# Optimization experiments

Measured on AMD Instinct MI355X. Metric: run time of the kernel, lower is better.

Reference implementation:

```python
import jax, jax.numpy as jnp
import numpy as np


def _lstm_scan(xs, W_ih, W_hh, b, h0, c0):
    """Run an LSTMCell over time. xs: [T, B, D]; returns (hs [T,B,H], h_T, c_T).
    PyTorch LSTMCell gate order: i, f, g, o; b = b_ih + b_hh fused."""
    H = h0.shape[-1]

    def step(carry, x_t):
        h, c = carry
        gates = x_t @ W_ih.T + h @ W_hh.T + b  # [B, 4H]
        i, f, g, o = jnp.split(gates, 4, axis=-1)
        i = jax.nn.sigmoid(i)
        f = jax.nn.sigmoid(f)
        g = jnp.tanh(g)
        o = jax.nn.sigmoid(o)
        c_new = f * c + i * g
        h_new = o * jnp.tanh(c_new)
        return (h_new, c_new), h_new

    (h_T, c_T), hs = jax.lax.scan(step, (h0, c0), xs)
    return hs, h_T, c_T


def setup_inputs() -> dict:
    key = jax.random.key(0)
    ks = jax.random.split(key, 7)
    B, T, F, H = 64, 512, 256, 1024
    s = lambda fan_in: np.sqrt(2.0) * np.sqrt(6.0 / (4 * H + fan_in))  # xavier_uniform gain=sqrt(2)
    return {
        "x": jax.random.normal(ks[0], (B, T, F), dtype=jnp.float32),
        "W_ih_e": jax.random.uniform(ks[1], (4 * H, F), jnp.float32, -s(F), s(F)),
        "W_hh_e": jax.random.uniform(ks[2], (4 * H, H), jnp.float32, -s(H), s(H)),
        "b_e": jnp.zeros((4 * H,), jnp.float32),
        "W_ih_d": jax.random.uniform(ks[3], (4 * H, H), jnp.float32, -s(H), s(H)),
        "W_hh_d": jax.random.uniform(ks[4], (4 * H, H), jnp.float32, -s(H), s(H)),
        "b_d": jnp.zeros((4 * H,), jnp.float32),
        "W_out": jax.random.uniform(ks[5], (F, H), jnp.float32, -s(F), s(F)),
        "b_out": jnp.zeros((F,), jnp.float32),
    }


def reference(x, W_ih_e, W_hh_e, b_e, W_ih_d, W_hh_d, b_d, W_out, b_out):
    B, T, F = x.shape
    H = W_hh_e.shape[1]
    xs = jnp.swapaxes(x, 0, 1)  # [T, B, F] time-major
    h0 = jnp.zeros((B, H), x.dtype)
    c0 = jnp.zeros((B, H), x.dtype)
    # Encoder: LSTMCell(F, H), collect per-step hidden states
    enc_hs, h_T, c_T = _lstm_scan(xs, W_ih_e, W_hh_e, b_e, h0, c0)  # [T, B, H]
    # Decoder: LSTMCell(H, H) over encoder hidden states, seeded with final (h, c)
    dec_hs, _, _ = _lstm_scan(enc_hs, W_ih_d, W_hh_d, b_d, h_T, c_T)  # [T, B, H]
    # Output projection H -> F
    out = jnp.einsum('tbh,fh->tbf', dec_hs, W_out) + b_out
    return jnp.swapaxes(out, 0, 1)  # [B, T, F]
```

## Files before the change

### kernel.cpp

```cpp
#include <hip/hip_runtime.h>
#include <math.h>

#define TT 512
#define BB 64
#define FF 256
#define HH 1024
#define NBLK 256
#define NCHE 5
#define NCHD 8

typedef __attribute__((ext_vector_type(8))) short short8;
typedef __attribute__((ext_vector_type(4))) float f32x4;

__device__ __forceinline__ unsigned short f2bf(float f) {
    unsigned u = __float_as_uint(f);
    u += 0x7FFFu + ((u >> 16) & 1u);
    return (unsigned short)(u >> 16);
}
__device__ __forceinline__ float bf2f(unsigned short u) {
    return __uint_as_float((unsigned)u << 16);
}

__global__ __launch_bounds__(256) void k_cast_x(const float* __restrict__ x,
                                                unsigned short* __restrict__ xB) {
    int t = blockIdx.x;
    #pragma unroll
    for (int i = 0; i < 16; ++i) {
        int id = threadIdx.x + i * 256;
        int b  = id >> 6;
        int f4 = (id & 63) << 2;
        float4 v = *(const float4*)(x + ((size_t)b * TT + t) * FF + f4);
        ushort4 o;
        o.x = f2bf(v.x); o.y = f2bf(v.y); o.z = f2bf(v.z); o.w = f2bf(v.w);
        *(ushort4*)(xB + ((size_t)t * BB + b) * FF + f4) = o;
    }
}

__global__ __launch_bounds__(256) void k_wcast(const float* __restrict__ in,
                                               unsigned short* __restrict__ out,
                                               int n4) {
    int stride = gridDim.x * 256;
    for (int i = blockIdx.x * 256 + threadIdx.x; i < n4; i += stride) {
        float4 v = ((const float4*)in)[i];
        ushort4 o;
        o.x = f2bf(v.x); o.y = f2bf(v.y); o.z = f2bf(v.z); o.w = f2bf(v.w);
        ((ushort4*)out)[i] = o;
    }
}

__device__ __forceinline__ void publish(unsigned* __restrict__ flags,
                                        int widx, unsigned val) {
    asm volatile("s_waitcnt vmcnt(0)" ::: "memory");
    if ((threadIdx.x & 63) == 0)
        __hip_atomic_store(flags + widx, val, __ATOMIC_RELAXED,
                           __HIP_MEMORY_SCOPE_AGENT);
}

__device__ __forceinline__ void waitall(const unsigned* __restrict__ flags,
                                        int lane, unsigned tgt) {
    const unsigned long long* f2 = (const unsigned long long*)flags;
    for (;;) {
        bool ok = true;
        #pragma unroll
        for (int k = 0; k < 8; ++k) {
            unsigned long long v = __hip_atomic_load(f2 + lane + 64 * k,
                                                     __ATOMIC_RELAXED,
                                                     __HIP_MEMORY_SCOPE_AGENT);
            ok &= ((unsigned)v >= tgt) && ((unsigned)(v >> 32) >= tgt);
        }
        if (__all(ok)) break;
        __builtin_amdgcn_s_sleep(2);
    }
    asm volatile("" ::: "memory");
}

template <int NCH, int NPRE>
__device__ __forceinline__ void lstm_step(
    const short8* __restrict__ sW,
    const unsigned short* __restrict__ A1, int K1,
    const unsigned short* __restrict__ A2, int K2, int C1,
    const f32x4 bias, float& creg,
    unsigned short* __restrict__ hOut,
    unsigned* __restrict__ flags, int tgt, int widx, unsigned pub,
    int lane, int q, int n, int j0, int u, int b)
{
    short8 av[3][8];
    auto aload = [&](short8* dst, int c) {
        const unsigned short* ap = (c < C1)
            ? A1 + (size_t)b * K1 + (size_t)c * 256
            : A2 + (size_t)b * K2 + (size_t)(c - C1) * 256;
        ap += q * 8;
        #pragma unroll
        for (int f = 0; f < 8; ++f) dst[f] = *(const short8*)(ap + f * 32);
    };

    aload(av[0], 0);
    if (NCH > 1 && NPRE > 1) aload(av[1], 1);

    if (tgt > 0) waitall(flags, lane, (unsigned)tgt);

    if (NCH > 1 && NPRE <= 1) aload(av[1], 1);

    f32x4 accA = {0.f, 0.f, 0.f, 0.f};
    f32x4 accB = {0.f, 0.f, 0.f, 0.f};
    #pragma unroll
    for (int c = 0; c < NCH; ++c) {
        if (c + 2 < NCH) aload(av[(c + 2) % 3], c + 2);
        const short8* cur = av[c % 3];
        #pragma unroll
        for (int f = 0; f < 8; ++f) {
            short8 wv = sW[(c * 8 + f) * 64 + lane];
            if (f & 1) accB = __builtin_amdgcn_mfma_f32_16x16x32_bf16(wv, cur[f], accB, 0, 0, 0);
            else       accA = __builtin_amdgcn_mfma_f32_16x16x32_bf16(wv, cur[f], accA, 0, 0, 0);
        }
    }
    f32x4 acc = accA + accB;

    float pi = acc[0] + bias[0];
    float pf = acc[1] + bias[1];
    float pg = acc[2] + bias[2];
    float po = acc[3] + bias[3];
    float iv = 1.f / (1.f + __expf(-pi));
    float fv = 1.f / (1.f + __expf(-pf));
    float gv = tanhf(pg);
    float ov = 1.f / (1.f + __expf(-po));
    float cn = fv * creg + iv * gv;
    creg = cn;
    float hn = ov * tanhf(cn);

    unsigned hv = (unsigned)f2bf(hn);
    unsigned v0 = (unsigned)__shfl((int)hv, n);
    unsigned v1 = (unsigned)__shfl((int)hv, n + 16);
    unsigned v2 = (unsigned)__shfl((int)hv, n + 32);
    unsigned v3 = (unsigned)__shfl((int)hv, n + 48);
    if (q == 0) {
        unsigned long long pk = (unsigned long long)(v0 | (v1 << 16)) |
                                ((unsigned long long)(v2 | (v3 << 16)) << 32);
        __hip_atomic_store((unsigned long long*)(hOut + (size_t)b * HH + j0), pk,
                           __ATOMIC_RELAXED, __HIP_MEMORY_SCOPE_AGENT);
    }
    if (pub) publish(flags, widx, pub);
}

__global__ __launch_bounds__(256, 1) void k_lstm_persist(
    const unsigned short* __restrict__ xB,
    const unsigned short* __restrict__ WihE,
    const unsigned short* __restrict__ WhhE,
    const float* __restrict__ bE,
    const unsigned short* __restrict__ WihD,
    const unsigned short* __restrict__ WhhD,
    const float* __restrict__ bD,
    unsigned short* __restrict__ encB,
    unsigned short* __restrict__ decR,
    unsigned* __restrict__ flags)
{
    __shared__ short8 sWe[NCHE * 8 * 64];
    __shared__ short8 sWd[NCHD * 8 * 64];

    const int tid  = threadIdx.x;
    const int lane = tid & 63;
    const int w    = tid >> 6;
    const int q    = lane >> 4;
    const int n    = lane & 15;
    const int j0   = blockIdx.x * 4;
    const int rrow = (n & 3) * HH + j0 + (n >> 2);
    const size_t SB = (size_t)BB * HH;
    const int widx = blockIdx.x * 4 + w;

    #pragma unroll
    for (int i = 0; i < 2 * NCHE; ++i) {
        int g = i * 4 + w;
        int c = g >> 3, f = g & 7;
        const unsigned short* Wp; int Ks; int cl;
        if (c < 1) { Wp = WihE; Ks = FF; cl = c; }
        else       { Wp = WhhE; Ks = HH; cl = c - 1; }
        sWe[g * 64 + lane] =
            *(const short8*)(Wp + (size_t)rrow * Ks + (size_t)cl * 256 + f * 32 + q * 8);
    }
    #pragma unroll
    for (int i = 0; i < 2 * NCHD; ++i) {
        int g = i * 4 + w;
        int c = g >> 3, f = g & 7;
        const unsigned short* Wp; int cl;
        if (c < 4) { Wp = WihD; cl = c; }
        else       { Wp = WhhD; cl = c - 4; }
        sWd[g * 64 + lane] =
            *(const short8*)(Wp + (size_t)rrow * HH + (size_t)cl * 256 + f * 32 + q * 8);
    }
    __syncthreads();

    const int u = j0 + q;
    const int b = w * 16 + n;
    const f32x4 biasE = {bE[u], bE[HH + u], bE[2 * HH + u], bE[3 * HH + u]};
    const f32x4 biasD = {bD[u], bD[HH + u], bD[2 * HH + u], bD[3 * HH + u]};

    float creg = 0.f;

    lstm_step<1, 1>(sWe, xB, FF, xB, FF, 1, biasE, creg,
                    encB, flags, 0, widx, 1u, lane, q, n, j0, u, b);
    for (int t = 1; t < TT; ++t) {
        lstm_step<NCHE, 1>(sWe, xB + (size_t)t * BB * FF, FF,
                           encB + (size_t)(t - 1) * SB, HH, 1,
                           biasE, creg, encB + (size_t)t * SB,
                           flags, t, widx, (unsigned)(t + 1),
                           lane, q, n, j0, u, b);
    }

    for (int t = 0; t < TT; ++t) {
        const unsigned short* A2 = (t == 0) ? encB + (size_t)(TT - 1) * SB
                                            : decR + (size_t)(t - 1) * SB;
        unsigned pub = (t == TT - 1) ? 0u : (unsigned)(TT + t + 1);
        lstm_step<NCHD, 2>(sWd, encB + (size_t)t * SB, HH, A2, HH, 4,
                           biasD, creg, decR + (size_t)t * SB,
                           flags, TT + t, widx, pub,
                           lane, q, n, j0, u, b);
    }
}

__global__ __launch_bounds__(256) void k_out_proj_r(
    const unsigned short* __restrict__ decR,
    const float* __restrict__ Wout,
    const float* __restrict__ bout,
    float* __restrict__ out)
{
    int t  = blockIdx.x;
    int fg = blockIdx.y;
    const int lane = threadIdx.x & 63;
    const int wv   = __builtin_amdgcn_readfirstlane(threadIdx.x >> 6);
    const int f0   = fg * 64 + wv * 16;
    const unsigned short* a = decR + ((size_t)t * BB + lane) * HH;

    float acc[16];
    #pragma unroll
    for (int i = 0; i < 16; ++i) acc[i] = bout[f0 + i];

    for (int k8 = 0; k8 < HH / 8; ++k8) {
        short8 hv8 = *(const short8*)(a + k8 * 8);
        #pragma unroll
        for (int uu = 0; uu < 8; ++uu) {
            float hv = bf2f((unsigned short)hv8[uu]);
            #pragma unroll
            for (int i = 0; i < 16; ++i)
                acc[i] = fmaf(Wout[(size_t)(f0 + i) * HH + k8 * 8 + uu], hv, acc[i]);
        }
    }

    float* op = out + ((size_t)lane * TT + t) * FF + f0;
    #pragma unroll
    for (int i = 0; i < 16; i += 4) {
        float4 v = make_float4(acc[i], acc[i + 1], acc[i + 2], acc[i + 3]);
        *(float4*)(op + i) = v;
    }
}

template <int NCH>
__global__ __launch_bounds__(256) void k_step_lds(
    const unsigned short* __restrict__ A1, const unsigned short* __restrict__ W1, int K1,
    const unsigned short* __restrict__ A2, const unsigned short* __restrict__ W2, int K2,
    int C1,
    const float* __restrict__ bias,
    float* __restrict__ Cbuf,
    unsigned short* __restrict__ hOut,
    float* __restrict__ chunkOut)
{
    __shared__ short8 sW[NCH * 8 * 64];

    const int tid  = threadIdx.x;
    const int lane = tid & 63;
    const int w    = tid >> 6;
    const int q    = lane >> 4;
    const int n    = lane & 15;
    const int j0   = blockIdx.x * 4;
    const int rrow = (n & 3) * HH + j0 + (n >> 2);

    short8 av[3][8];

    auto aload = [&](short8* dst, int c) {
        const unsigned short* ap = (c < C1)
            ? A1 + (size_t)(w * 16 + n) * K1 + (size_t)c * 256
            : A2 + (size_t)(w * 16 + n) * K2 + (size_t)(c - C1) * 256;
        ap += q * 8;
        #pragma unroll
        for (int f = 0; f < 8; ++f) dst[f] = *(const short8*)(ap + f * 32);
    };

    aload(av[0], 0);
    if (NCH > 1) aload(av[1], 1);

    #pragma unroll
    for (int i = 0; i < 2 * NCH; ++i) {
        int g = i * 4 + w;
        int c = g >> 3, f = g & 7;
        const unsigned short* Wp; int Ks; int cl;
        if (c < C1) { Wp = W1; Ks = K1; cl = c; }
        else        { Wp = W2; Ks = K2; cl = c - C1; }
        sW[g * 64 + lane] =
            *(const short8*)(Wp + (size_t)rrow * Ks + (size_t)cl * 256 + f * 32 + q * 8);
    }
    __syncthreads();

    f32x4 accA = {0.f, 0.f, 0.f, 0.f};
    f32x4 accB = {0.f, 0.f, 0.f, 0.f};
    #pragma unroll
    for (int c = 0; c < NCH; ++c) {
        if (c + 2 < NCH) aload(av[(c + 2) % 3], c + 2);
        const short8* cur = av[c % 3];
        #pragma unroll
        for (int f = 0; f < 8; ++f) {
            short8 wv = sW[(c * 8 + f) * 64 + lane];
            if (f & 1) accB = __builtin_amdgcn_mfma_f32_16x16x32_bf16(wv, cur[f], accB, 0, 0, 0);
            else       accA = __builtin_amdgcn_mfma_f32_16x16x32_bf16(wv, cur[f], accA, 0, 0, 0);
        }
    }
    f32x4 acc = accA + accB;

    const int u = j0 + q;
    const int b = w * 16 + n;
    float pi = acc[0] + bias[u];
    float pf = acc[1] + bias[HH + u];
    float pg = acc[2] + bias[2 * HH + u];
    float po = acc[3] + bias[3 * HH + u];
    float iv = 1.f / (1.f + __expf(-pi));
    float fv = 1.f / (1.f + __expf(-pf));
    float gv = tanhf(pg);
    float ov = 1.f / (1.f + __expf(-po));
    size_t cix = (size_t)u * BB + b;
    float c  = Cbuf[cix];
    float cn = fv * c + iv * gv;
    Cbuf[cix] = cn;
    float hn = ov * tanhf(cn);
    hOut[(size_t)b * HH + u] = f2bf(hn);
    if (chunkOut) chunkOut[cix] = hn;
}

__device__ __forceinline__ void seg_f32(const unsigned short* __restrict__ ap0,
                                        const float* __restrict__ wp0,
                                        int nch, f32x4& acc) {
    const unsigned short* ap = ap0;
    const float* wp = wp0;
    #pragma unroll 2
    for (int c = 0; c < nch; ++c) {
        float4 wa = *(const float4*)wp;
        float4 wb = *(const float4*)(wp + 4);
        short8 av = *(const short8*)ap;
        short8 wv;
        wv[0] = (short)f2bf(wa.x); wv[1] = (short)f2bf(wa.y);
        wv[2] = (short)f2bf(wa.z); wv[3] = (short)f2bf(wa.w);
        wv[4] = (short)f2bf(wb.x); wv[5] = (short)f2bf(wb.y);
        wv[6] = (short)f2bf(wb.z); wv[7] = (short)f2bf(wb.w);
        acc = __builtin_amdgcn_mfma_f32_16x16x32_bf16(wv, av, acc, 0, 0, 0);
        ap += 32; wp += 32;
    }
}

__global__ __launch_bounds__(256) void k_step_f32w(
    const unsigned short* __restrict__ A1, const float* __restrict__ W1, int K1,
    const unsigned short* __restrict__ A2, const float* __restrict__ W2, int K2,
    const float* __restrict__ bias,
    float* __restrict__ Cbuf, unsigned short* __restrict__ hOut,
    float* __restrict__ chunkOut)
{
    const int tid  = threadIdx.x;
    const int lane = tid & 63;
    const int w    = tid >> 6;
    const int q    = lane >> 4;
    const int n    = lane & 15;
    const int j0   = blockIdx.x * 4;
    const int rrow = (n & 3) * HH + j0 + (n >> 2);

    f32x4 acc = {0.f, 0.f, 0.f, 0.f};
    seg_f32(A1 + (size_t)(w * 16 + n) * K1 + q * 8,
            W1 + (size_t)rrow * K1 + q * 8, K1 >> 5, acc);
    if (K2)
        seg_f32(A2 + (size_t)(w * 16 + n) * HH + q * 8,
                W2 + (size_t)rrow * HH + q * 8, HH >> 5, acc);

    const int u = j0 + q;
    const int b = w * 16 + n;
    float pi = acc[0] + bias[u];
    float pf = acc[1] + bias[HH + u];
    float pg = acc[2] + bias[2 * HH + u];
    float po = acc[3] + bias[3 * HH + u];
    float iv = 1.f / (1.f + __expf(-pi));
    float fv = 1.f / (1.f + __expf(-pf));
    float gv = tanhf(pg);
    float ov = 1.f / (1.f + __expf(-po));
    size_t cix = (size_t)u * BB + b;
    float c  = Cbuf[cix];
    float cn = fv * c + iv * gv;
    Cbuf[cix] = cn;
    float hn = ov * tanhf(cn);
    hOut[(size_t)b * HH + u] = f2bf(hn);
    if (chunkOut) chunkOut[cix] = hn;
}

__global__ __launch_bounds__(256) void k_out_proj(
    const float* __restrict__ chunk,
    const float* __restrict__ Wout,
    const float* __restrict__ bout,
    float* __restrict__ out,
    int t0)
{
    int tl = blockIdx.x;
    int t  = t0 + tl;
    int fg = blockIdx.y;
    const int lane = threadIdx.x & 63;
    const int wv   = __builtin_amdgcn_readfirstlane(threadIdx.x >> 6);
    const int f0   = fg * 64 + wv * 16;
    const float* a = chunk + (size_t)tl * HH * BB;

    float acc[16];
    #pragma unroll
    for (int i = 0; i < 16; ++i) acc[i] = bout[f0 + i];

    for (int k = 0; k < HH; k += 4) {
        #pragma unroll
        for (int u = 0; u < 4; ++u) {
            float hv = a[(size_t)(k + u) * BB + lane];
            #pragma unroll
            for (int i = 0; i < 16; ++i)
                acc[i] = fmaf(Wout[(size_t)(f0 + i) * HH + k + u], hv, acc[i]);
        }
    }

    float* op = out + ((size_t)lane * TT + t) * FF + f0;
    #pragma unroll
    for (int i = 0; i < 16; i += 4) {
        float4 v = make_float4(acc[i], acc[i + 1], acc[i + 2], acc[i + 3]);
        *(float4*)(op + i) = v;
    }
}

extern "C" void kernel_launch(void* const* d_in, const int* in_sizes, int n_in,
                              void* d_out, int out_size, void* d_ws, size_t ws_size,
                              hipStream_t stream) {
    const float* x     = (const float*)d_in[0];
    const float* Wih_e = (const float*)d_in[1];
    const float* Whh_e = (const float*)d_in[2];
    const float* b_e   = (const float*)d_in[3];
    const float* Wih_d = (const float*)d_in[4];
    const float* Whh_d = (const float*)d_in[5];
    const float* b_d   = (const float*)d_in[6];
    const float* Wout  = (const float*)d_in[7];
    const float* bout  = (const float*)d_in[8];
    float* out = (float*)d_out;

    const size_t SB = (size_t)BB * HH;

    unsigned short* xB = (unsigned short*)d_out;

    {
        char* p = (char*)d_ws;
        unsigned* flags = (unsigned*)p; p += 4096;
        unsigned short* encB  = (unsigned short*)p; p += (size_t)TT * SB * 2;
        unsigned short* decR  = (unsigned short*)p; p += (size_t)TT * SB * 2;
        unsigned short* WihEb = (unsigned short*)p; p += (size_t)4 * HH * FF * 2;
        unsigned short* WhhEb = (unsigned short*)p; p += (size_t)4 * HH * HH * 2;
        unsigned short* WihDb = (unsigned short*)p; p += (size_t)4 * HH * HH * 2;
        unsigned short* WhhDb = (unsigned short*)p; p += (size_t)4 * HH * HH * 2;
        size_t need = (size_t)(p - (char*)d_ws);

        if (ws_size >= need) {
            hipMemsetAsync(flags, 0, 4096, stream);
            k_cast_x<<<TT, 256, 0, stream>>>(x, xB);
            k_wcast<<<1024, 256, 0, stream>>>(Wih_e, WihEb, 4 * HH * FF / 4);
            k_wcast<<<1024, 256, 0, stream>>>(Whh_e, WhhEb, 4 * HH * HH / 4);
            k_wcast<<<1024, 256, 0, stream>>>(Wih_d, WihDb, 4 * HH * HH / 4);
            k_wcast<<<1024, 256, 0, stream>>>(Whh_d, WhhDb, 4 * HH * HH / 4);

            void* args[] = {
                (void*)&xB, (void*)&WihEb, (void*)&WhhEb, (void*)&b_e,
                (void*)&WihDb, (void*)&WhhDb, (void*)&b_d,
                (void*)&encB, (void*)&decR, (void*)&flags};
            hipLaunchCooperativeKernel((const void*)k_lstm_persist,
                                       dim3(NBLK), dim3(256), args, 0, stream);

            k_out_proj_r<<<dim3(TT, 4), 256, 0, stream>>>(decR, Wout, bout, out);
            return;
        }
    }

    char* p = (char*)d_ws;
    unsigned short* encB  = (unsigned short*)p; p += (size_t)TT * SB * 2;
    unsigned short* dech0 = (unsigned short*)p; p += SB * 2;
    unsigned short* dech1 = (unsigned short*)p; p += SB * 2;
    float* cbuf = (float*)p; p += SB * 4;
    size_t used  = (size_t)(p - (char*)d_ws);
    size_t avail = ws_size > used ? ws_size - used : 0;

    const size_t WE_B = ((size_t)4 * HH * FF + (size_t)4 * HH * HH) * 2;
    const size_t WD_B = ((size_t)4 * HH * HH) * 2 * 2;
    const size_t CH8  = (size_t)8 * SB * 4;

    bool wbAll = (avail >= WE_B + WD_B + CH8);
    bool wbEnc = wbAll || (avail >= WE_B + CH8);

    unsigned short *WihEb = 0, *WhhEb = 0, *WihDb = 0, *WhhDb = 0;
    if (wbEnc) {
        WihEb = (unsigned short*)p; p += (size_t)4 * HH * FF * 2;
        WhhEb = (unsigned short*)p; p += (size_t)4 * HH * HH * 2;
        avail -= WE_B;
    }
    if (wbAll) {
        WihDb = (unsigned short*)p; p += (size_t)4 * HH * HH * 2;
        WhhDb = (unsigned short*)p; p += (size_t)4 * HH * HH * 2;
        avail -= WD_B;
    }
    int C = 8;
    if      (avail >= (size_t)64 * SB * 4) C = 64;
    else if (avail >= (size_t)32 * SB * 4) C = 32;
    else if (avail >= (size_t)16 * SB * 4) C = 16;
    float* chunk = (float*)p;

    hipMemsetAsync(cbuf, 0, SB * 4, stream);
    k_cast_x<<<TT, 256, 0, stream>>>(x, xB);
    if (wbEnc) {
        k_wcast<<<1024, 256, 0, stream>>>(Wih_e, WihEb, 4 * HH * FF / 4);
        k_wcast<<<1024, 256, 0, stream>>>(Whh_e, WhhEb, 4 * HH * HH / 4);
    }
    if (wbAll) {
        k_wcast<<<1024, 256, 0, stream>>>(Wih_d, WihDb, 4 * HH * HH / 4);
        k_wcast<<<1024, 256, 0, stream>>>(Whh_d, WhhDb, 4 * HH * HH / 4);
    }

    for (int t = 0; t < TT; ++t) {
        const unsigned short* A1 = xB + (size_t)t * BB * FF;
        const unsigned short* A2 = t ? encB + (size_t)(t - 1) * SB : (unsigned short*)0;
        unsigned short* hOut = encB + (size_t)t * SB;
        if (wbEnc) {
            if (t == 0)
                k_step_lds<1><<<256, 256, 0, stream>>>(A1, WihEb, FF, A2, WhhEb, HH,
                                                       1, b_e, cbuf, hOut, (float*)0);
            else
                k_step_lds<5><<<256, 256, 0, stream>>>(A1, WihEb, FF, A2, WhhEb, HH,
                                                       1, b_e, cbuf, hOut, (float*)0);
        } else {
            k_step_f32w<<<256, 256, 0, stream>>>(A1, Wih_e, FF, A2, Whh_e,
                                                 t ? HH : 0, b_e, cbuf, hOut, (float*)0);
        }
    }

    for (int t = 0; t < TT; ++t) {
        const unsigned short* A1 = encB + (size_t)t * SB;
        const unsigned short* A2 = (t == 0) ? encB + (size_t)(TT - 1) * SB
                                            : ((t & 1) ? dech1 : dech0);
        unsigned short* hOut = ((t + 1) & 1) ? dech1 : dech0;
        int l = t & (C - 1);
        float* ch = chunk + (size_t)l * SB;
        if (wbAll)
            k_step_lds<8><<<256, 256, 0, stream>>>(A1, WihDb, HH, A2, WhhDb, HH,
                                                   4, b_d, cbuf, hOut, ch);
        else
            k_step_f32w<<<256, 256, 0, stream>>>(A1, Wih_d, FF, A2, Whh_d, HH,
                                                 b_d, cbuf, hOut, ch);
        if (l == C - 1)
            k_out_proj<<<dim3(C, 4), 256, 0, stream>>>(chunk, Wout, bout, out,
                                                       t - (C - 1));
    }
}
```

Measured before the change: 12.05 ms.

## Add hierarchical flag aggregation and compute input-side MFMAs before barrier wait

Each block gains a fifth warp. In every 16th block that warp acts as an aggregator: it watches 64 per-warp progress flags and writes the combined epoch into 8 mirrored pages. Compute warps then poll one small mirror line instead of scanning all 1024 flags. The lstm_step also runs all input-dependent MFMA chunks (x for the encoder, encoder hidden state for the decoder) before waiting on the barrier, overlapping that work with the sync. The trade-off is an extra relay hop of latency per step and extra resident warps.

```diff
diff --git a/kernel.cpp b/kernel.cpp
--- a/kernel.cpp
+++ b/kernel.cpp
@@ -56,32 +56,48 @@
                            __HIP_MEMORY_SCOPE_AGENT);
 }
 
-__device__ __forceinline__ void waitall(const unsigned* __restrict__ flags,
-                                        int lane, unsigned tgt) {
-    const unsigned long long* f2 = (const unsigned long long*)flags;
+__device__ __forceinline__ void waitall16(const unsigned* __restrict__ mir,
+                                          int mpage, int lane, unsigned tgt) {
+    const unsigned long long* line =
+        (const unsigned long long*)(mir + mpage * 64);
     for (;;) {
-        bool ok = true;
-        #pragma unroll
-        for (int k = 0; k < 8; ++k) {
-            unsigned long long v = __hip_atomic_load(f2 + lane + 64 * k,
-                                                     __ATOMIC_RELAXED,
-                                                     __HIP_MEMORY_SCOPE_AGENT);
-            ok &= ((unsigned)v >= tgt) && ((unsigned)(v >> 32) >= tgt);
-        }
+        unsigned long long v = __hip_atomic_load(line + (lane & 7),
+                                                 __ATOMIC_RELAXED,
+                                                 __HIP_MEMORY_SCOPE_AGENT);
+        bool ok = ((unsigned)v >= tgt) && ((unsigned)(v >> 32) >= tgt);
         if (__all(ok)) break;
-        __builtin_amdgcn_s_sleep(2);
+        __builtin_amdgcn_s_sleep(1);
     }
     asm volatile("" ::: "memory");
 }
 
-template <int NCH, int NPRE>
+__device__ __forceinline__ void aggregator(unsigned* __restrict__ flags,
+                                           unsigned* __restrict__ mir,
+                                           int g, int lane) {
+    for (unsigned e = 1; e <= 2u * TT - 1; ++e) {
+        for (;;) {
+            unsigned v = __hip_atomic_load(flags + g * 64 + lane,
+                                           __ATOMIC_RELAXED,
+                                           __HIP_MEMORY_SCOPE_AGENT);
+            if (__all(v >= e)) break;
+            __builtin_amdgcn_s_sleep(1);
+        }
+        if (lane < 8)
+            __hip_atomic_store(mir + lane * 64 + g, e, __ATOMIC_RELAXED,
+                               __HIP_MEMORY_SCOPE_AGENT);
+        asm volatile("s_waitcnt vmcnt(0)" ::: "memory");
+    }
+}
+
+template <int NCH, int C1>
 __device__ __forceinline__ void lstm_step(
     const short8* __restrict__ sW,
     const unsigned short* __restrict__ A1, int K1,
-    const unsigned short* __restrict__ A2, int K2, int C1,
+    const unsigned short* __restrict__ A2, int K2,
     const f32x4 bias, float& creg,
     unsigned short* __restrict__ hOut,
-    unsigned* __restrict__ flags, int tgt, int widx, unsigned pub,
+    unsigned* __restrict__ flags, unsigned* __restrict__ mir,
+    int tgt, int widx, unsigned pub, int mpage,
     int lane, int q, int n, int j0, int u, int b)
 {
     short8 av[3][8];
@@ -94,24 +110,38 @@
         for (int f = 0; f < 8; ++f) dst[f] = *(const short8*)(ap + f * 32);
     };
 
-    aload(av[0], 0);
-    if (NCH > 1 && NPRE > 1) aload(av[1], 1);
-
-    if (tgt > 0) waitall(flags, lane, (unsigned)tgt);
-
-    if (NCH > 1 && NPRE <= 1) aload(av[1], 1);
-
     f32x4 accA = {0.f, 0.f, 0.f, 0.f};
     f32x4 accB = {0.f, 0.f, 0.f, 0.f};
-    #pragma unroll
-    for (int c = 0; c < NCH; ++c) {
-        if (c + 2 < NCH) aload(av[(c + 2) % 3], c + 2);
+
+    aload(av[0], 0);
+    if (C1 > 1) aload(av[1], 1);
+    #pragma unroll
+    for (int c = 0; c < C1; ++c) {
+        if (c + 2 < C1) aload(av[(c + 2) % 3], c + 2);
         const short8* cur = av[c % 3];
         #pragma unroll
         for (int f = 0; f < 8; ++f) {
             short8 wv = sW[(c * 8 + f) * 64 + lane];
             if (f & 1) accB = __builtin_amdgcn_mfma_f32_16x16x32_bf16(wv, cur[f], accB, 0, 0, 0);
             else       accA = __builtin_amdgcn_mfma_f32_16x16x32_bf16(wv, cur[f], accA, 0, 0, 0);
+        }
+    }
+
+    if (tgt > 0) waitall16(mir, mpage, lane, (unsigned)tgt);
+
+    if (NCH > C1) {
+        aload(av[C1 % 3], C1);
+        if (NCH > C1 + 1) aload(av[(C1 + 1) % 3], C1 + 1);
+        #pragma unroll
+        for (int c = C1; c < NCH; ++c) {
+            if (c + 2 < NCH) aload(av[(c + 2) % 3], c + 2);
+            const short8* cur = av[c % 3];
+            #pragma unroll
+            for (int f = 0; f < 8; ++f) {
+                short8 wv = sW[(c * 8 + f) * 64 + lane];
+                if (f & 1) accB = __builtin_amdgcn_mfma_f32_16x16x32_bf16(wv, cur[f], accB, 0, 0, 0);
+                else       accA = __builtin_amdgcn_mfma_f32_16x16x32_bf16(wv, cur[f], accA, 0, 0, 0);
+            }
         }
     }
     f32x4 acc = accA + accB;
@@ -142,7 +172,7 @@
     if (pub) publish(flags, widx, pub);
 }
 
-__global__ __launch_bounds__(256, 1) void k_lstm_persist(
+__global__ __launch_bounds__(320, 1) void k_lstm_persist(
     const unsigned short* __restrict__ xB,
     const unsigned short* __restrict__ WihE,
     const unsigned short* __restrict__ WhhE,
@@ -160,12 +190,22 @@
     const int tid  = threadIdx.x;
     const int lane = tid & 63;
     const int w    = tid >> 6;
+    unsigned* mir  = flags + 1024;
+
+    if (w == 4) {
+        __syncthreads();
+        if ((blockIdx.x & 15) == 0)
+            aggregator(flags, mir, blockIdx.x >> 4, lane);
+        return;
+    }
+
     const int q    = lane >> 4;
     const int n    = lane & 15;
     const int j0   = blockIdx.x * 4;
     const int rrow = (n & 3) * HH + j0 + (n >> 2);
     const size_t SB = (size_t)BB * HH;
-    const int widx = blockIdx.x * 4 + w;
+    const int widx  = blockIdx.x * 4 + w;
+    const int mpage = blockIdx.x & 7;
 
     #pragma unroll
     for (int i = 0; i < 2 * NCHE; ++i) {
@@ -196,13 +236,14 @@
 
     float creg = 0.f;
 
-    lstm_step<1, 1>(sWe, xB, FF, xB, FF, 1, biasE, creg,
-                    encB, flags, 0, widx, 1u, lane, q, n, j0, u, b);
+    lstm_step<1, 1>(sWe, xB, FF, xB, FF, biasE, creg,
+                    encB, flags, mir, 0, widx, 1u, mpage,
+                    lane, q, n, j0, u, b);
     for (int t = 1; t < TT; ++t) {
         lstm_step<NCHE, 1>(sWe, xB + (size_t)t * BB * FF, FF,
-                           encB + (size_t)(t - 1) * SB, HH, 1,
+                           encB + (size_t)(t - 1) * SB, HH,
                            biasE, creg, encB + (size_t)t * SB,
-                           flags, t, widx, (unsigned)(t + 1),
+                           flags, mir, t, widx, (unsigned)(t + 1), mpage,
                            lane, q, n, j0, u, b);
     }
 
@@ -210,9 +251,9 @@
         const unsigned short* A2 = (t == 0) ? encB + (size_t)(TT - 1) * SB
                                             : decR + (size_t)(t - 1) * SB;
         unsigned pub = (t == TT - 1) ? 0u : (unsigned)(TT + t + 1);
-        lstm_step<NCHD, 2>(sWd, encB + (size_t)t * SB, HH, A2, HH, 4,
+        lstm_step<NCHD, 4>(sWd, encB + (size_t)t * SB, HH, A2, HH,
                            biasD, creg, decR + (size_t)t * SB,
-                           flags, TT + t, widx, pub,
+                           flags, mir, TT + t, widx, pub, mpage,
                            lane, q, n, j0, u, b);
     }
 }
@@ -451,7 +492,7 @@
 
     {
         char* p = (char*)d_ws;
-        unsigned* flags = (unsigned*)p; p += 4096;
+        unsigned* flags = (unsigned*)p; p += 8192;
         unsigned short* encB  = (unsigned short*)p; p += (size_t)TT * SB * 2;
         unsigned short* decR  = (unsigned short*)p; p += (size_t)TT * SB * 2;
         unsigned short* WihEb = (unsigned short*)p; p += (size_t)4 * HH * FF * 2;
@@ -461,7 +502,7 @@
         size_t need = (size_t)(p - (char*)d_ws);
 
         if (ws_size >= need) {
-            hipMemsetAsync(flags, 0, 4096, stream);
+            hipMemsetAsync(flags, 0, 8192, stream);
             k_cast_x<<<TT, 256, 0, stream>>>(x, xB);
             k_wcast<<<1024, 256, 0, stream>>>(Wih_e, WihEb, 4 * HH * FF / 4);
             k_wcast<<<1024, 256, 0, stream>>>(Whh_e, WhhEb, 4 * HH * HH / 4);
@@ -473,7 +514,7 @@
                 (void*)&WihDb, (void*)&WhhDb, (void*)&b_d,
                 (void*)&encB, (void*)&decR, (void*)&flags};
             hipLaunchCooperativeKernel((const void*)k_lstm_persist,
-                                       dim3(NBLK), dim3(256), args, 0, stream);
+                                       dim3(NBLK), dim3(320), args, 0, stream);
 
             k_out_proj_r<<<dim3(TT, 4), 256, 0, stream>>>(decR, Wout, bout, out);
             return;
```

Result: faster. 10.41 ms (-13.6%).
